# Kernel tuning notes

Measured on AMD Instinct MI355X. Metric: run time of the kernel, lower is better.

Reference implementation:

```python
import jax, jax.numpy as jnp
import numpy as np

B, N, IN_DIM, OUT_DIM, H = 4, 2048, 1024, 1024, 16
HEAD_DIM = OUT_DIM // H  # 64


def setup_inputs() -> dict:
    key = jax.random.key(0)
    k_x, k_q, k_k, k_v, k_o = jax.random.split(key, 5)
    s = 1.0 / np.sqrt(IN_DIM)
    return {
        "x": jax.random.normal(k_x, (B, N, IN_DIM), dtype=jnp.float32),
        "w_q": jax.random.normal(k_q, (IN_DIM, OUT_DIM), dtype=jnp.float32) * s,
        "w_k": jax.random.normal(k_k, (IN_DIM, OUT_DIM), dtype=jnp.float32) * s,
        "w_v": jax.random.normal(k_v, (IN_DIM, OUT_DIM), dtype=jnp.float32) * s,
        "w_out": jax.random.normal(k_o, (OUT_DIM, OUT_DIM), dtype=jnp.float32) * s,
    }


def reference(x, w_q, w_k, w_v, w_out):
    b, n, _ = x.shape
    scale = 1.0 / jnp.sqrt(jnp.float32(HEAD_DIM))
    # QKV projections, split into heads: [b, h, n, d]
    q = (x @ w_q).reshape(b, n, H, HEAD_DIM).transpose(0, 2, 1, 3)
    k = (x @ w_k).reshape(b, n, H, HEAD_DIM).transpose(0, 2, 1, 3)
    v = (x @ w_v).reshape(b, n, H, HEAD_DIM).transpose(0, 2, 1, 3)
    # full score matrix [b, h, q, k]
    scores = jnp.einsum("bhqd,bhkd->bhqk", q, k) * scale
    # NOTE: source applies softmax over dim=1 (the HEAD axis) — reproduce exactly
    attn = jax.nn.softmax(scores, axis=1)
    # dropout p=0.0 -> identity
    ctx = jnp.einsum("bhqk,bhkd->bqhd", attn, v).reshape(b, n, OUT_DIM)
    return ctx @ w_out
```

## Files before the change

kernel.cpp:

```cpp
#include <hip/hip_runtime.h>
#include <hip/hip_bf16.h>

typedef unsigned short u16;
typedef unsigned int u32;
typedef __attribute__((ext_vector_type(8))) short short8;
typedef __attribute__((ext_vector_type(4))) float float4v;
typedef __attribute__((ext_vector_type(4))) unsigned int uint4v;

__device__ __forceinline__ u16 f2bf(float f) {
    union { float f; unsigned int u; } v; v.f = f;
    unsigned int r = v.u + 0x7fffu + ((v.u >> 16) & 1u);
    return (u16)(r >> 16);
}

__device__ __forceinline__ u32 cvtpk(float lo, float hi) {
    u32 r;
    asm("v_cvt_pk_bf16_f32 %0, %1, %2" : "=v"(r) : "v"(lo), "v"(hi));
    return r;
}

__device__ __forceinline__ void gld_lds16(const u16* g, u16* l) {
    __builtin_amdgcn_global_load_lds(
        (const __attribute__((address_space(1))) u32*)g,
        (__attribute__((address_space(3))) u32*)l, 16, 0, 0);
}

__global__ __launch_bounds__(256) void convert_x(
    const float* __restrict__ x, u16* __restrict__ xb) {
    int i = (blockIdx.x * 256 + threadIdx.x) * 8;
    float4v a = *(const float4v*)&x[i];
    float4v b = *(const float4v*)&x[i + 4];
    u16 tmp[8] __attribute__((aligned(16)));
#pragma unroll
    for (int j = 0; j < 4; ++j) { tmp[j] = f2bf(a[j]); tmp[4 + j] = f2bf(b[j]); }
    *(uint4v*)&xb[i] = *(uint4v*)tmp;
}

__global__ __launch_bounds__(256) void transpose_w(
    const float* __restrict__ w0, const float* __restrict__ w1,
    const float* __restrict__ w2, const float* __restrict__ w3,
    u16* __restrict__ o0, u16* __restrict__ o1,
    u16* __restrict__ o2, u16* __restrict__ o3) {
    __shared__ u16 t[32][33];
    int z = blockIdx.z;
    const float* w = (z == 0) ? w0 : (z == 1) ? w1 : (z == 2) ? w2 : w3;
    u16* o         = (z == 0) ? o0 : (z == 1) ? o1 : (z == 2) ? o2 : o3;
    int bx = blockIdx.x * 32;
    int by = blockIdx.y * 32;
    int x = threadIdx.x, y = threadIdx.y;
#pragma unroll
    for (int i = 0; i < 4; ++i)
        t[y + i * 8][x] = f2bf(w[(size_t)(by + y + i * 8) * 1024 + bx + x]);
    __syncthreads();
#pragma unroll
    for (int i = 0; i < 4; ++i)
        o[(size_t)(bx + y + i * 8) * 1024 + by + x] = t[x][y + i * 8];
}

__global__ __launch_bounds__(256) void gemm_bt(
    const u16* __restrict__ A, const u16* __restrict__ Bt,
    void* __restrict__ Cout, int M, int N, int K, int mode, float oscale) {
    __shared__ __attribute__((aligned(16))) u16 As[128 * 32];
    __shared__ __attribute__((aligned(16))) u16 Bs[128 * 32];
    const int tid = threadIdx.x;
    const int m0 = blockIdx.y * 128;
    const int n0 = blockIdx.x * 128;
    const int wid = tid >> 6;
    const int lane = tid & 63;
    const int ln = lane & 15, kq = lane >> 4;
    const int wm = (wid >> 1) * 64, wn = (wid & 1) * 64;

    float4v acc[4][4] = {};
    for (int k0 = 0; k0 < K; k0 += 32) {
#pragma unroll
        for (int i = 0; i < 2; ++i) {
            int chunk = tid + i * 256;
            int row = chunk >> 2, cg = chunk & 3;
            u16* lA = &As[(size_t)(i * 256 + wid * 64) * 8];
            u16* lB = &Bs[(size_t)(i * 256 + wid * 64) * 8];
            gld_lds16(&A[(size_t)(m0 + row) * K + k0 + cg * 8], lA);
            gld_lds16(&Bt[(size_t)(n0 + row) * K + k0 + cg * 8], lB);
        }
        __syncthreads();
        short8 af[4], bfr[4];
#pragma unroll
        for (int mt = 0; mt < 4; ++mt)
            af[mt] = *(const short8*)&As[(wm + mt * 16 + ln) * 32 + kq * 8];
#pragma unroll
        for (int nt = 0; nt < 4; ++nt)
            bfr[nt] = *(const short8*)&Bs[(wn + nt * 16 + ln) * 32 + kq * 8];
#pragma unroll
        for (int mt = 0; mt < 4; ++mt)
#pragma unroll
            for (int nt = 0; nt < 4; ++nt)
                acc[mt][nt] = __builtin_amdgcn_mfma_f32_16x16x32_bf16(
                    af[mt], bfr[nt], acc[mt][nt], 0, 0, 0);
        __syncthreads();
    }
    if (mode == 0) {
        u16* C = (u16*)Cout;
#pragma unroll
        for (int mt = 0; mt < 4; ++mt)
#pragma unroll
            for (int nt = 0; nt < 4; ++nt)
#pragma unroll
                for (int r = 0; r < 4; ++r) {
                    int row = m0 + wm + mt * 16 + kq * 4 + r;
                    int col = n0 + wn + nt * 16 + ln;
                    C[(size_t)row * N + col] = f2bf(acc[mt][nt][r] * oscale);
                }
    } else if (mode == 1) {
        u16* C = (u16*)Cout;
#pragma unroll
        for (int mt = 0; mt < 4; ++mt)
#pragma unroll
            for (int nt = 0; nt < 4; ++nt)
#pragma unroll
                for (int r = 0; r < 4; ++r) {
                    int t = m0 + wm + mt * 16 + kq * 4 + r;
                    int col = n0 + wn + nt * 16 + ln;
                    int b = t >> 11, n = t & 2047;
                    C[((size_t)(b * 1024 + col)) * 2048 + n] = f2bf(acc[mt][nt][r]);
                }
    } else {
        float* C = (float*)Cout;
#pragma unroll
        for (int mt = 0; mt < 4; ++mt)
#pragma unroll
            for (int nt = 0; nt < 4; ++nt)
#pragma unroll
                for (int r = 0; r < 4; ++r) {
                    int row = m0 + wm + mt * 16 + kq * 4 + r;
                    int col = n0 + wn + nt * 16 + ln;
                    C[(size_t)row * N + col] = acc[mt][nt][r];
                }
    }
}

__global__ __launch_bounds__(1024) void attn_kernel(
    const u16* qb, const u16* __restrict__ kb,
    const u16* __restrict__ vt, u16* cb) {
    __shared__ __attribute__((aligned(16))) float Ef[2][512 * 36];
    __shared__ __attribute__((aligned(16))) float Di[32 * 36];

    const int b = blockIdx.y;
    const int q0 = blockIdx.x * 32;
    const int tid = threadIdx.x;
    const int wid = tid >> 6, lane = tid & 63;
    const int ln = lane & 15, kq = lane >> 4;
    const int h = wid;

    short8 aq[2][2];
#pragma unroll
    for (int mt = 0; mt < 2; ++mt)
#pragma unroll
        for (int kc = 0; kc < 2; ++kc)
            aq[mt][kc] = *(const short8*)&qb[
                (size_t)(b * 2048 + q0 + mt * 16 + ln) * 1024 +
                h * 64 + kc * 32 + kq * 8];

    float4v cacc[2][4] = {};

#pragma unroll 1
    for (int kt = 0; kt < 2048; kt += 32) {
        const int cur = (kt >> 5) & 1;
        float* E = Ef[cur];

        short8 bk[2][2];
#pragma unroll
        for (int kc = 0; kc < 2; ++kc)
#pragma unroll
            for (int nt = 0; nt < 2; ++nt)
                bk[kc][nt] = *(const short8*)&kb[
                    (size_t)(b * 2048 + kt + nt * 16 + ln) * 1024 +
                    h * 64 + kc * 32 + kq * 8];

        float4v sacc[2][2] = {};
#pragma unroll
        for (int kc = 0; kc < 2; ++kc)
#pragma unroll
            for (int mt = 0; mt < 2; ++mt)
#pragma unroll
                for (int nt = 0; nt < 2; ++nt)
                    sacc[mt][nt] = __builtin_amdgcn_mfma_f32_16x16x32_bf16(
                        bk[kc][nt], aq[mt][kc], sacc[mt][nt], 0, 0, 0);

#pragma unroll
        for (int mt = 0; mt < 2; ++mt)
#pragma unroll
            for (int nt = 0; nt < 2; ++nt) {
                float4v e;
#pragma unroll
                for (int r = 0; r < 4; ++r)
                    e[r] = exp2f(fminf(sacc[mt][nt][r], 115.0f));
                *(float4v*)&E[(h * 32 + mt * 16 + ln) * 36 + nt * 16 + kq * 4] = e;
            }

        short8 bv[4];
#pragma unroll
        for (int nt = 0; nt < 4; ++nt)
            bv[nt] = *(const short8*)&vt[
                (size_t)(b * 1024 + h * 64 + nt * 16 + ln) * 2048 + kt + kq * 8];

        __syncthreads();

        {
            const int q = tid >> 5, kk = tid & 31;
            const float* ec = &E[q * 36 + kk];
            float d0 = 0.f, d1 = 0.f, d2 = 0.f, d3 = 0.f;
#pragma unroll
            for (int hh = 0; hh < 4; ++hh) {
                d0 += ec[(hh * 4 + 0) * (32 * 36)];
                d1 += ec[(hh * 4 + 1) * (32 * 36)];
                d2 += ec[(hh * 4 + 2) * (32 * 36)];
                d3 += ec[(hh * 4 + 3) * (32 * 36)];
            }
            Di[q * 36 + kk] = __builtin_amdgcn_rcpf((d0 + d1) + (d2 + d3));
        }
        __syncthreads();

        short8 ap[2];
#pragma unroll
        for (int mt = 0; mt < 2; ++mt) {
            const float* ep = &E[(h * 32 + mt * 16 + ln) * 36 + kq * 8];
            const float* dp = &Di[(mt * 16 + ln) * 36 + kq * 8];
            float4v e0 = *(const float4v*)&ep[0];
            float4v e1 = *(const float4v*)&ep[4];
            float4v g0 = *(const float4v*)&dp[0];
            float4v g1 = *(const float4v*)&dp[4];
            u32 pk[4] __attribute__((aligned(16)));
            pk[0] = cvtpk(e0[0] * g0[0], e0[1] * g0[1]);
            pk[1] = cvtpk(e0[2] * g0[2], e0[3] * g0[3]);
            pk[2] = cvtpk(e1[0] * g1[0], e1[1] * g1[1]);
            pk[3] = cvtpk(e1[2] * g1[2], e1[3] * g1[3]);
            ap[mt] = *(short8*)pk;
        }
#pragma unroll
        for (int nt = 0; nt < 4; ++nt)
#pragma unroll
            for (int mt = 0; mt < 2; ++mt)
                cacc[mt][nt] = __builtin_amdgcn_mfma_f32_16x16x32_bf16(
                    ap[mt], bv[nt], cacc[mt][nt], 0, 0, 0);
    }

#pragma unroll
    for (int mt = 0; mt < 2; ++mt)
#pragma unroll
        for (int nt = 0; nt < 4; ++nt)
#pragma unroll
            for (int r = 0; r < 4; ++r) {
                int row = b * 2048 + q0 + mt * 16 + kq * 4 + r;
                int col = h * 64 + nt * 16 + ln;
                cb[(size_t)row * 1024 + col] = f2bf(cacc[mt][nt][r]);
            }
}

extern "C" void kernel_launch(void* const* d_in, const int* in_sizes, int n_in,
                              void* d_out, int out_size, void* d_ws, size_t ws_size,
                              hipStream_t stream) {
    const float* x   = (const float*)d_in[0];
    const float* w_q = (const float*)d_in[1];
    const float* w_k = (const float*)d_in[2];
    const float* w_v = (const float*)d_in[3];
    const float* w_o = (const float*)d_in[4];

    char* ws = (char*)d_ws;
    const size_t SZ_W   = (size_t)1024 * 1024 * 2;
    const size_t SZ_TOK = (size_t)8192 * 1024 * 2;
    u16* x_bf  = (u16*)(ws);
    u16* wtq   = (u16*)(ws + SZ_TOK);
    u16* wtk   = (u16*)(ws + SZ_TOK + SZ_W);
    u16* wtv   = (u16*)(ws + SZ_TOK + 2 * SZ_W);
    u16* wto   = (u16*)(ws + SZ_TOK + 3 * SZ_W);
    u16* q_buf = (u16*)(ws + SZ_TOK + 4 * SZ_W);
    u16* k_buf  = (u16*)d_out;
    u16* vt_buf = (u16*)d_out + (size_t)8192 * 1024;

    convert_x<<<4096, 256, 0, stream>>>(x, x_bf);

    transpose_w<<<dim3(32, 32, 4), dim3(32, 8), 0, stream>>>(
        w_q, w_k, w_v, w_o, wtq, wtk, wtv, wto);

    gemm_bt<<<dim3(8, 64), 256, 0, stream>>>(x_bf, wtq, q_buf, 8192, 1024, 1024, 0, 0.18033688f);
    gemm_bt<<<dim3(8, 64), 256, 0, stream>>>(x_bf, wtk, k_buf, 8192, 1024, 1024, 0, 1.0f);
    gemm_bt<<<dim3(8, 64), 256, 0, stream>>>(x_bf, wtv, vt_buf, 8192, 1024, 1024, 1, 1.0f);

    attn_kernel<<<dim3(64, 4), 1024, 0, stream>>>(q_buf, k_buf, vt_buf, q_buf);

    gemm_bt<<<dim3(8, 64), 256, 0, stream>>>(q_buf, wto, d_out, 8192, 1024, 1024, 2, 1.0f);
}
```

Before: 494.4 us.

## Software-pipeline attention stages across iterations with bf16 exp buffer and one barrier

Restructures the attention loop into a three-stage software pipeline: QK^T+exp for tile i, head-sum reciprocal for tile i-1, and PV MFMA for tile i-2 all run in one iteration separated by a single __syncthreads instead of two. The exp values are stored in LDS as bf16, halving that buffer, and the buffer is triple-buffered. V loads are prefetched one iteration ahead in registers. The head reduction now runs on a quarter of the threads with vector reads. This cuts barrier count and LDS traffic at the cost of extra registers and an added bf16 rounding of exp before normalization.

```diff
diff --git a/kernel.cpp b/kernel.cpp
--- a/kernel.cpp
+++ b/kernel.cpp
@@ -6,6 +6,7 @@
 typedef __attribute__((ext_vector_type(8))) short short8;
 typedef __attribute__((ext_vector_type(4))) float float4v;
 typedef __attribute__((ext_vector_type(4))) unsigned int uint4v;
+typedef __attribute__((ext_vector_type(2))) unsigned int uint2v;
 
 __device__ __forceinline__ u16 f2bf(float f) {
     union { float f; unsigned int u; } v; v.f = f;
@@ -17,6 +18,12 @@
     u32 r;
     asm("v_cvt_pk_bf16_f32 %0, %1, %2" : "=v"(r) : "v"(lo), "v"(hi));
     return r;
+}
+__device__ __forceinline__ float bflo(u32 u) {
+    union { u32 u; float f; } v; v.u = u << 16; return v.f;
+}
+__device__ __forceinline__ float bfhi(u32 u) {
+    union { u32 u; float f; } v; v.u = u & 0xffff0000u; return v.f;
 }
 
 __device__ __forceinline__ void gld_lds16(const u16* g, u16* l) {
@@ -137,11 +144,11 @@
     }
 }
 
-__global__ __launch_bounds__(1024) void attn_kernel(
+__global__ __launch_bounds__(1024, 4) void attn_kernel(
     const u16* qb, const u16* __restrict__ kb,
     const u16* __restrict__ vt, u16* cb) {
-    __shared__ __attribute__((aligned(16))) float Ef[2][512 * 36];
-    __shared__ __attribute__((aligned(16))) float Di[32 * 36];
+    __shared__ __attribute__((aligned(16))) u16   Ebuf[3][512 * 36];
+    __shared__ __attribute__((aligned(16))) float Dibuf[2][32 * 36];
 
     const int b = blockIdx.y;
     const int q0 = blockIdx.x * 32;
@@ -160,87 +167,98 @@
                 h * 64 + kc * 32 + kq * 8];
 
     float4v cacc[2][4] = {};
-
+    short8 bvA[4], bvB[4];
+
+    const int NT = 64;
 #pragma unroll 1
-    for (int kt = 0; kt < 2048; kt += 32) {
-        const int cur = (kt >> 5) & 1;
-        float* E = Ef[cur];
-
+    for (int i = 0; i < NT + 2; ++i) {
         short8 bk[2][2];
-#pragma unroll
-        for (int kc = 0; kc < 2; ++kc)
-#pragma unroll
-            for (int nt = 0; nt < 2; ++nt)
-                bk[kc][nt] = *(const short8*)&kb[
-                    (size_t)(b * 2048 + kt + nt * 16 + ln) * 1024 +
-                    h * 64 + kc * 32 + kq * 8];
-
-        float4v sacc[2][2] = {};
-#pragma unroll
-        for (int kc = 0; kc < 2; ++kc)
+        if (i < NT) {
+            const int kt = i * 32;
+#pragma unroll
+            for (int kc = 0; kc < 2; ++kc)
+#pragma unroll
+                for (int nt = 0; nt < 2; ++nt)
+                    bk[kc][nt] = *(const short8*)&kb[
+                        (size_t)(b * 2048 + kt + nt * 16 + ln) * 1024 +
+                        h * 64 + kc * 32 + kq * 8];
+        }
+        if (i >= 1 && i <= NT) {
+            const int kt = (i - 1) * 32;
+#pragma unroll
+            for (int nt = 0; nt < 4; ++nt)
+                bvB[nt] = *(const short8*)&vt[
+                    (size_t)(b * 1024 + h * 64 + nt * 16 + ln) * 2048 + kt + kq * 8];
+        }
+        if (i >= 2) {
+            const u16*   Ee = Ebuf[(i - 2) % 3];
+            const float* Dd = Dibuf[(i - 2) & 1];
+            short8 ap[2];
+#pragma unroll
+            for (int mt = 0; mt < 2; ++mt) {
+                const u16* ep = &Ee[(h * 32 + mt * 16 + ln) * 36 + kq * 8];
+                uint2v ea = *(const uint2v*)&ep[0];
+                uint2v eb = *(const uint2v*)&ep[4];
+                const float* dp = &Dd[(mt * 16 + ln) * 36 + kq * 8];
+                float4v g0 = *(const float4v*)&dp[0];
+                float4v g1 = *(const float4v*)&dp[4];
+                u32 pk[4] __attribute__((aligned(16)));
+                pk[0] = cvtpk(bflo(ea[0]) * g0[0], bfhi(ea[0]) * g0[1]);
+                pk[1] = cvtpk(bflo(ea[1]) * g0[2], bfhi(ea[1]) * g0[3]);
+                pk[2] = cvtpk(bflo(eb[0]) * g1[0], bfhi(eb[0]) * g1[1]);
+                pk[3] = cvtpk(bflo(eb[1]) * g1[2], bfhi(eb[1]) * g1[3]);
+                ap[mt] = *(short8*)pk;
+            }
+#pragma unroll
+            for (int nt = 0; nt < 4; ++nt)
+#pragma unroll
+                for (int mt = 0; mt < 2; ++mt)
+                    cacc[mt][nt] = __builtin_amdgcn_mfma_f32_16x16x32_bf16(
+                        ap[mt], bvA[nt], cacc[mt][nt], 0, 0, 0);
+        }
+        if (i < NT) {
+            float4v sacc[2][2] = {};
+#pragma unroll
+            for (int kc = 0; kc < 2; ++kc)
+#pragma unroll
+                for (int mt = 0; mt < 2; ++mt)
+#pragma unroll
+                    for (int nt = 0; nt < 2; ++nt)
+                        sacc[mt][nt] = __builtin_amdgcn_mfma_f32_16x16x32_bf16(
+                            bk[kc][nt], aq[mt][kc], sacc[mt][nt], 0, 0, 0);
+            u16* Ew = Ebuf[i % 3];
 #pragma unroll
             for (int mt = 0; mt < 2; ++mt)
 #pragma unroll
-                for (int nt = 0; nt < 2; ++nt)
-                    sacc[mt][nt] = __builtin_amdgcn_mfma_f32_16x16x32_bf16(
-                        bk[kc][nt], aq[mt][kc], sacc[mt][nt], 0, 0, 0);
-
-#pragma unroll
-        for (int mt = 0; mt < 2; ++mt)
-#pragma unroll
-            for (int nt = 0; nt < 2; ++nt) {
-                float4v e;
-#pragma unroll
-                for (int r = 0; r < 4; ++r)
-                    e[r] = exp2f(fminf(sacc[mt][nt][r], 115.0f));
-                *(float4v*)&E[(h * 32 + mt * 16 + ln) * 36 + nt * 16 + kq * 4] = e;
+                for (int nt = 0; nt < 2; ++nt) {
+                    float e0 = exp2f(fminf(sacc[mt][nt][0], 115.0f));
+                    float e1 = exp2f(fminf(sacc[mt][nt][1], 115.0f));
+                    float e2 = exp2f(fminf(sacc[mt][nt][2], 115.0f));
+                    float e3 = exp2f(fminf(sacc[mt][nt][3], 115.0f));
+                    uint2v w; w[0] = cvtpk(e0, e1); w[1] = cvtpk(e2, e3);
+                    *(uint2v*)&Ew[(h * 32 + mt * 16 + ln) * 36 + nt * 16 + kq * 4] = w;
+                }
+        }
+        if (i >= 1 && i <= NT && tid < 256) {
+            const u16* Ee = Ebuf[(i - 1) % 3];
+            const int q = tid >> 3, k4 = tid & 7;
+            float d0 = 0.f, d1 = 0.f, d2 = 0.f, d3 = 0.f;
+#pragma unroll
+            for (int hh = 0; hh < 16; ++hh) {
+                uint2v e = *(const uint2v*)&Ee[(hh * 32 + q) * 36 + k4 * 4];
+                d0 += bflo(e[0]); d1 += bfhi(e[0]);
+                d2 += bflo(e[1]); d3 += bfhi(e[1]);
             }
-
-        short8 bv[4];
-#pragma unroll
-        for (int nt = 0; nt < 4; ++nt)
-            bv[nt] = *(const short8*)&vt[
-                (size_t)(b * 1024 + h * 64 + nt * 16 + ln) * 2048 + kt + kq * 8];
-
+            float4v dv;
+            dv[0] = __builtin_amdgcn_rcpf(d0);
+            dv[1] = __builtin_amdgcn_rcpf(d1);
+            dv[2] = __builtin_amdgcn_rcpf(d2);
+            dv[3] = __builtin_amdgcn_rcpf(d3);
+            *(float4v*)&Dibuf[(i - 1) & 1][q * 36 + k4 * 4] = dv;
+        }
         __syncthreads();
-
-        {
-            const int q = tid >> 5, kk = tid & 31;
-            const float* ec = &E[q * 36 + kk];
-            float d0 = 0.f, d1 = 0.f, d2 = 0.f, d3 = 0.f;
-#pragma unroll
-            for (int hh = 0; hh < 4; ++hh) {
-                d0 += ec[(hh * 4 + 0) * (32 * 36)];
-                d1 += ec[(hh * 4 + 1) * (32 * 36)];
-                d2 += ec[(hh * 4 + 2) * (32 * 36)];
-                d3 += ec[(hh * 4 + 3) * (32 * 36)];
-            }
-            Di[q * 36 + kk] = __builtin_amdgcn_rcpf((d0 + d1) + (d2 + d3));
-        }
-        __syncthreads();
-
-        short8 ap[2];
-#pragma unroll
-        for (int mt = 0; mt < 2; ++mt) {
-            const float* ep = &E[(h * 32 + mt * 16 + ln) * 36 + kq * 8];
-            const float* dp = &Di[(mt * 16 + ln) * 36 + kq * 8];
-            float4v e0 = *(const float4v*)&ep[0];
-            float4v e1 = *(const float4v*)&ep[4];
-            float4v g0 = *(const float4v*)&dp[0];
-            float4v g1 = *(const float4v*)&dp[4];
-            u32 pk[4] __attribute__((aligned(16)));
-            pk[0] = cvtpk(e0[0] * g0[0], e0[1] * g0[1]);
-            pk[1] = cvtpk(e0[2] * g0[2], e0[3] * g0[3]);
-            pk[2] = cvtpk(e1[0] * g1[0], e1[1] * g1[1]);
-            pk[3] = cvtpk(e1[2] * g1[2], e1[3] * g1[3]);
-            ap[mt] = *(short8*)pk;
-        }
-#pragma unroll
-        for (int nt = 0; nt < 4; ++nt)
-#pragma unroll
-            for (int mt = 0; mt < 2; ++mt)
-                cacc[mt][nt] = __builtin_amdgcn_mfma_f32_16x16x32_bf16(
-                    ap[mt], bv[nt], cacc[mt][nt], 0, 0, 0);
+#pragma unroll
+        for (int nt = 0; nt < 4; ++nt) bvA[nt] = bvB[nt];
     }
 
 #pragma unroll
```

After: 536.5 us. +8.5%, slower.

## Split attention key range across two blocks and combine with bf16 atomics

Applied to the files above, without the earlier changes.

The attention kernel grid grows from 256 to 512 blocks, and each block handles half of the key sequence. Partial context results are merged with packed bf16 atomic adds into a buffer that is zeroed first, reusing the x_bf workspace. The goal is better CU occupancy, since 256 blocks underfill the GPU. The cost is an extra zeroing kernel, atomic traffic, and bf16 rounding when the two halves are accumulated.

```diff
diff --git a/kernel.cpp b/kernel.cpp
--- a/kernel.cpp
+++ b/kernel.cpp
@@ -34,6 +34,11 @@
 #pragma unroll
     for (int j = 0; j < 4; ++j) { tmp[j] = f2bf(a[j]); tmp[4 + j] = f2bf(b[j]); }
     *(uint4v*)&xb[i] = *(uint4v*)tmp;
+}
+
+__global__ __launch_bounds__(256) void zero_buf(uint4v* __restrict__ p) {
+    uint4v z = {0u, 0u, 0u, 0u};
+    p[(size_t)blockIdx.x * 256 + threadIdx.x] = z;
 }
 
 __global__ __launch_bounds__(256) void transpose_w(
@@ -138,13 +143,16 @@
 }
 
 __global__ __launch_bounds__(1024) void attn_kernel(
-    const u16* qb, const u16* __restrict__ kb,
-    const u16* __restrict__ vt, u16* cb) {
+    const u16* __restrict__ qb, const u16* __restrict__ kb,
+    const u16* __restrict__ vt, u16* __restrict__ ctx) {
     __shared__ __attribute__((aligned(16))) float Ef[2][512 * 36];
     __shared__ __attribute__((aligned(16))) float Di[32 * 36];
 
-    const int b = blockIdx.y;
-    const int q0 = blockIdx.x * 32;
+    const int bx = blockIdx.x;
+    const int qt = bx >> 3;
+    const int slot = bx & 7;
+    const int b = slot >> 1, kh = slot & 1;
+    const int q0 = qt * 32;
     const int tid = threadIdx.x;
     const int wid = tid >> 6, lane = tid & 63;
     const int ln = lane & 15, kq = lane >> 4;
@@ -162,8 +170,9 @@
     float4v cacc[2][4] = {};
 
 #pragma unroll 1
-    for (int kt = 0; kt < 2048; kt += 32) {
-        const int cur = (kt >> 5) & 1;
+    for (int t = 0; t < 32; ++t) {
+        const int kt = (kh << 10) + (t << 5);
+        const int cur = t & 1;
         float* E = Ef[cur];
 
         short8 bk[2][2];
@@ -249,9 +258,17 @@
         for (int nt = 0; nt < 4; ++nt)
 #pragma unroll
             for (int r = 0; r < 4; ++r) {
-                int row = b * 2048 + q0 + mt * 16 + kq * 4 + r;
-                int col = h * 64 + nt * 16 + ln;
-                cb[(size_t)row * 1024 + col] = f2bf(cacc[mt][nt][r]);
+                union { float f; int i; } v; v.f = cacc[mt][nt][r];
+                int pv = __builtin_amdgcn_ds_swizzle(v.i, 0x041F);
+                if (!(lane & 1)) {
+                    union { int i; float f; } pw; pw.i = pv;
+                    u32 d = cvtpk(v.f, pw.f);
+                    int row = b * 2048 + q0 + mt * 16 + kq * 4 + r;
+                    int col = h * 64 + nt * 16 + ln;
+                    u16* p = &ctx[(size_t)row * 1024 + col];
+                    asm volatile("global_atomic_pk_add_bf16 %0, %1, off"
+                                 :: "v"(p), "v"(d) : "memory");
+                }
             }
 }
 
@@ -273,6 +290,7 @@
     u16* wtv   = (u16*)(ws + SZ_TOK + 2 * SZ_W);
     u16* wto   = (u16*)(ws + SZ_TOK + 3 * SZ_W);
     u16* q_buf = (u16*)(ws + SZ_TOK + 4 * SZ_W);
+    u16* ctx   = x_bf;
     u16* k_buf  = (u16*)d_out;
     u16* vt_buf = (u16*)d_out + (size_t)8192 * 1024;
 
@@ -285,7 +303,9 @@
     gemm_bt<<<dim3(8, 64), 256, 0, stream>>>(x_bf, wtk, k_buf, 8192, 1024, 1024, 0, 1.0f);
     gemm_bt<<<dim3(8, 64), 256, 0, stream>>>(x_bf, wtv, vt_buf, 8192, 1024, 1024, 1, 1.0f);
 
-    attn_kernel<<<dim3(64, 4), 1024, 0, stream>>>(q_buf, k_buf, vt_buf, q_buf);
-
-    gemm_bt<<<dim3(8, 64), 256, 0, stream>>>(q_buf, wto, d_out, 8192, 1024, 1024, 2, 1.0f);
-}
+    zero_buf<<<4096, 256, 0, stream>>>((uint4v*)ctx);
+
+    attn_kernel<<<dim3(512), 1024, 0, stream>>>(q_buf, k_buf, vt_buf, ctx);
+
+    gemm_bt<<<dim3(8, 64), 256, 0, stream>>>(ctx, wto, d_out, 8192, 1024, 1024, 2, 1.0f);
+}
```

Measured after the change: 547.0 us. 10.6% more time.
